# Kernel optimization log

Hardware: AMD Instinct MI355X
Metric: run time of the kernel (lower is better)

Reference implementation:

```python
import jax, jax.numpy as jnp
import numpy as np

B, S, D = 1, 1024, 512
HEADS, HID = 8, 64
DH = D // HEADS          # 64
CD = D * DH              # 32768 channels in diagonal block
DT = 0.1


def causal_fft_conv(u, k):
    # u: (..., C, S), k: (C, S) -> causal convolution along last axis
    s = u.shape[-1]
    n = 2 * s
    Uf = jnp.fft.rfft(u, n=n, axis=-1)
    Kf = jnp.fft.rfft(k, n=n, axis=-1)
    return jnp.fft.irfft(Uf * Kf, n=n, axis=-1)[..., :s]


def setup_inputs() -> dict:
    key = jax.random.key(0)
    ks = jax.random.split(key, 10)
    x = jax.random.normal(ks[0], (B, S, D), dtype=jnp.float32)
    sc = 1.0 / np.sqrt(D)
    WQ = jax.random.normal(ks[1], (D, D), dtype=jnp.float32) * sc
    WK = jax.random.normal(ks[2], (D, D), dtype=jnp.float32) * sc
    WV = jax.random.normal(ks[3], (D, D), dtype=jnp.float32) * sc
    WO = jax.random.normal(ks[4], (D, D), dtype=jnp.float32) * sc
    # shift SSM: taps C (A = shift matrix, B = e1) + skip D
    C_shift = jax.random.normal(ks[5], (D, HID), dtype=jnp.float32) / np.sqrt(HID)
    D_shift = jax.random.normal(ks[6], (D,), dtype=jnp.float32)
    # S4D-Inv initialization (deterministic: real_random=imag_random=False)
    n = np.arange(HID, dtype=np.float32)
    A_re = jnp.full((HID,), -0.5, dtype=jnp.float32)
    A_im = jnp.asarray((HID / np.pi) * (HID / (2.0 * n + 1.0) - 1.0), dtype=jnp.float32)
    C_re = jax.random.normal(ks[7], (CD, HID), dtype=jnp.float32) / np.sqrt(HID)
    C_im = jax.random.normal(ks[8], (CD, HID), dtype=jnp.float32) / np.sqrt(HID)
    D_diag = jax.random.normal(ks[9], (CD,), dtype=jnp.float32)
    return {"x": x, "WQ": WQ, "WK": WK, "WV": WV, "WO": WO,
            "C_shift": C_shift, "D_shift": D_shift,
            "A_re": A_re, "A_im": A_im, "C_re": C_re, "C_im": C_im,
            "D_diag": D_diag}


def reference(x, WQ, WK, WV, WO, C_shift, D_shift, A_re, A_im, C_re, C_im, D_diag):
    b, s, d = x.shape
    Q = x @ WQ.T
    K = x @ WK.T
    V = x @ WV.T

    # ---- S4 shift block on K: FIR conv with taps C_shift + skip ----
    k_shift = jnp.pad(C_shift, ((0, 0), (0, s - HID)))  # (D, S)
    Kc = jnp.swapaxes(K, 1, 2)                          # (B, D, S)
    Kc = causal_fft_conv(Kc, k_shift) + D_shift[:, None] * Kc
    K = jnp.swapaxes(Kc, 1, 2)

    # ---- heads ----
    Qh = jnp.swapaxes(Q.reshape(b, s, HEADS, DH), 1, 2)  # (B,H,S,dh)
    Kh = jnp.swapaxes(K.reshape(b, s, HEADS, DH), 1, 2)
    Vh = jnp.swapaxes(V.reshape(b, s, HEADS, DH), 1, 2)

    # KV outer product: (B,H,S,dh,dh)
    KV = Kh[..., :, None] * Vh[..., None, :]
    KVf = jnp.transpose(KV, (0, 2, 1, 3, 4)).reshape(b, s, CD)

    # ---- S4D diagonal block (bilinear disc., convolutional form) ----
    A = A_re + 1j * A_im                                # (N,) complex
    dA = (1.0 + DT * A / 2.0) / (1.0 - DT * A / 2.0)
    dB = DT / (1.0 - DT * A / 2.0)
    logdA = jnp.log(dA)                                 # (N,)
    vand = jnp.exp(jnp.arange(s)[None, :] * logdA[:, None])  # (N, S)
    CB = (C_re + 1j * C_im) * dB[None, :]               # (CD, N)
    Kd = 2.0 * jnp.real(CB @ vand)                      # (CD, S) SSM kernel

    KVc = jnp.swapaxes(KVf, 1, 2)                       # (B, CD, S)
    KVc = causal_fft_conv(KVc, Kd) + D_diag[:, None] * KVc
    KVd = jnp.swapaxes(KVc, 1, 2).reshape(b, s, HEADS, DH, DH)
    KVd = jnp.transpose(KVd, (0, 2, 1, 3, 4))           # (B,H,S,dh,dh)

    # ---- combine with Q and output projection ----
    O = jnp.einsum('bhnc,bhncd->bhnd', Qh, KVd)         # (B,H,S,dh)
    O = jnp.swapaxes(O, 1, 2).reshape(b, s, d)
    return O @ WO.T
```

## Files before the change

### kernel.cpp

```cpp
#include <hip/hip_runtime.h>

#define S 1024
#define D 512
#define HID 64
#define CD 32768
#define DT 0.1f

typedef __attribute__((ext_vector_type(4))) float floatx4;
typedef __attribute__((ext_vector_type(8))) short shortx8;
typedef short shortx8_a __attribute__((ext_vector_type(8), may_alias));
typedef short shortx4_a __attribute__((ext_vector_type(4), may_alias));
typedef unsigned int uint_a __attribute__((may_alias));
typedef unsigned int uint2_a __attribute__((ext_vector_type(2), may_alias));
typedef float float4_a __attribute__((ext_vector_type(4), may_alias));
typedef float float_a __attribute__((may_alias));

__device__ __forceinline__ unsigned short f2bf(float f) {
  union { float f; unsigned int u; } v;
  v.f = f;
  unsigned int r = v.u + 0x7FFFu + ((v.u >> 16) & 1u);
  return (unsigned short)(r >> 16);
}
__device__ __forceinline__ float bf2f(unsigned short h) {
  union { unsigned int u; float f; } v;
  v.u = ((unsigned int)h) << 16;
  return v.f;
}
__device__ __forceinline__ void cvt_hilo(float v, unsigned short& h, unsigned short& lo) {
  h = f2bf(v);
  lo = f2bf(v - bf2f(h));
}

__global__ __launch_bounds__(256) void fused_qkv_cbkd(
    const float* __restrict__ x, const float* __restrict__ WQ,
    const float* __restrict__ WK, const float* __restrict__ WV,
    const float* __restrict__ Are, const float* __restrict__ Aim,
    const float* __restrict__ Cre, const float* __restrict__ Cim,
    float* __restrict__ QT, float* __restrict__ KrawT, float* __restrict__ VT,
    unsigned short* __restrict__ cb2pack, unsigned short* __restrict__ kdpack) {
  __shared__ __align__(16) char LB[21760];
  const int tid = threadIdx.x;
  const int bid = blockIdx.x;
  const int l = tid & 63, w = tid >> 6;
  const int l15 = l & 15, q = l >> 4;

  if (bid < 384) {
    unsigned short* Wh = (unsigned short*)LB;
    unsigned short* Wl = Wh + 2560;
    unsigned short* Xh = Wl + 2560;
    unsigned short* Xl = Xh + 2560;
    float_a* Ct = (float_a*)LB;
    const int mat = bid >> 7;
    const int rem = bid & 127;
    const int n0 = (rem & 7) * 64, m0 = (rem >> 3) * 64;
    const float* Wsel = (mat == 0) ? WQ : (mat == 1) ? WK : WV;
    float* CT = (mat == 0) ? QT : (mat == 1) ? KrawT : VT;

    floatx4 acc[4];
#pragma unroll
    for (int nt = 0; nt < 4; ++nt) acc[nt] = (floatx4){0.f, 0.f, 0.f, 0.f};

    for (int k0 = 0; k0 < D; k0 += 32) {
      if (k0) __syncthreads();
#pragma unroll
      for (int p = 0; p < 2; ++p) {
        const int idx = tid + 256 * p;
        const int row = idx >> 3, c4 = (idx & 7) * 4;
        const float4 wv = *(const float4*)&Wsel[(n0 + row) * D + k0 + c4];
        const float4 xv = *(const float4*)&x[(m0 + row) * D + k0 + c4];
        unsigned short h0, h1, h2, h3, g0, g1, g2, g3;
        cvt_hilo(wv.x, h0, g0); cvt_hilo(wv.y, h1, g1);
        cvt_hilo(wv.z, h2, g2); cvt_hilo(wv.w, h3, g3);
        uint2_a hv = {(unsigned int)h0 | ((unsigned int)h1 << 16),
                      (unsigned int)h2 | ((unsigned int)h3 << 16)};
        uint2_a lv = {(unsigned int)g0 | ((unsigned int)g1 << 16),
                      (unsigned int)g2 | ((unsigned int)g3 << 16)};
        *(uint2_a*)&Wh[row * 40 + c4] = hv;
        *(uint2_a*)&Wl[row * 40 + c4] = lv;
        cvt_hilo(xv.x, h0, g0); cvt_hilo(xv.y, h1, g1);
        cvt_hilo(xv.z, h2, g2); cvt_hilo(xv.w, h3, g3);
        uint2_a hv2 = {(unsigned int)h0 | ((unsigned int)h1 << 16),
                       (unsigned int)h2 | ((unsigned int)h3 << 16)};
        uint2_a lv2 = {(unsigned int)g0 | ((unsigned int)g1 << 16),
                       (unsigned int)g2 | ((unsigned int)g3 << 16)};
        *(uint2_a*)&Xh[row * 40 + c4] = hv2;
        *(uint2_a*)&Xl[row * 40 + c4] = lv2;
      }
      __syncthreads();
      const shortx8 xh = *(const shortx8_a*)&Xh[(16 * w + l15) * 40 + 8 * q];
      const shortx8 xl = *(const shortx8_a*)&Xl[(16 * w + l15) * 40 + 8 * q];
#pragma unroll
      for (int nt = 0; nt < 4; ++nt) {
        const shortx8 wh = *(const shortx8_a*)&Wh[(16 * nt + l15) * 40 + 8 * q];
        const shortx8 wl = *(const shortx8_a*)&Wl[(16 * nt + l15) * 40 + 8 * q];
        acc[nt] = __builtin_amdgcn_mfma_f32_16x16x32_bf16(wh, xh, acc[nt], 0, 0, 0);
        acc[nt] = __builtin_amdgcn_mfma_f32_16x16x32_bf16(wh, xl, acc[nt], 0, 0, 0);
        acc[nt] = __builtin_amdgcn_mfma_f32_16x16x32_bf16(wl, xh, acc[nt], 0, 0, 0);
      }
    }
    __syncthreads();
#pragma unroll
    for (int nt = 0; nt < 4; ++nt)
#pragma unroll
      for (int v = 0; v < 4; ++v)
        Ct[(16 * nt + 4 * q + v) * 68 + 16 * w + l15] = acc[nt][v];
    __syncthreads();
#pragma unroll
    for (int p = 0; p < 4; ++p) {
      const int row = (tid >> 4) + 16 * p;
      const int col4 = (tid & 15) * 4;
      *(float4_a*)&CT[(n0 + row) * S + m0 + col4] = *(const float4_a*)&Ct[row * 68 + col4];
    }
  } else {
    unsigned short* cbs = (unsigned short*)LB;
    unsigned short* PCc2s = (unsigned short*)(LB + 4352);
    const int c0 = (bid - 384) << 4;
    {
      const int n = l, seg = w;
      const float ar = Are[n], ai = Aim[n];
      const float den_re = 1.0f - 0.05f * ar;
      const float den_im = -0.05f * ai;
      const float num_re = 1.0f + 0.05f * ar;
      const float num_im = 0.05f * ai;
      const float inv_d2 = 1.0f / (den_re * den_re + den_im * den_im);
      const float dAr = (num_re * den_re + num_im * den_im) * inv_d2;
      const float dAi = (num_im * den_re - num_re * den_im) * inv_d2;
      float e2r = dAr * dAr - dAi * dAi, e2i = 2.0f * dAr * dAi;
      float e4r = e2r * e2r - e2i * e2i, e4i = 2.0f * e2r * e2i;
      float e8r = e4r * e4r - e4i * e4i, e8i = 2.0f * e4r * e4i;
      float e16r = e8r * e8r - e8i * e8i, e16i = 2.0f * e8r * e8i;
      float br = 1.0f, bi = 0.0f;
      for (int sgo = 0; sgo < seg; ++sgo) {
        const float nr = br * e16r - bi * e16i;
        bi = br * e16i + bi * e16r;
        br = nr;
      }
      float pr = br, pi = bi;
      for (int k = 16 * seg + 1; k <= 16 * seg + 16; ++k) {
        const float nr = pr * dAr - pi * dAi;
        pi = pr * dAi + pi * dAr;
        pr = nr;
        if (k <= 63) {
          PCc2s[k * 136 + n] = f2bf(pr);
          PCc2s[k * 136 + 64 + n] = f2bf(-pi);
        }
      }
      if (seg == 0) {
        PCc2s[n] = f2bf(1.0f);
        PCc2s[64 + n] = 0;
      }
    }
#pragma unroll
    for (int ii = 0; ii < 4; ++ii) {
      const int idx = tid + 256 * ii;
      const int ci = idx >> 6, n = idx & 63;
      const int c = c0 + ci;
      const float ar = Are[n], ai = Aim[n];
      const float den_re = 1.0f - 0.05f * ar;
      const float den_im = -0.05f * ai;
      const float inv_d2 = 1.0f / (den_re * den_re + den_im * den_im);
      const float dBr = DT * den_re * inv_d2;
      const float dBi = -DT * den_im * inv_d2;
      const float cr = Cre[c * HID + n], cim = Cim[c * HID + n];
      const unsigned short re = f2bf(2.0f * (cr * dBr - cim * dBi));
      const unsigned short im = f2bf(2.0f * (cr * dBi + cim * dBr));
      cbs[ci * 136 + n] = re;
      cbs[ci * 136 + 64 + n] = im;
      cb2pack[c * 128 + n] = re;
      cb2pack[c * 128 + 64 + n] = im;
    }
    __syncthreads();
    floatx4 acc = {0.f, 0.f, 0.f, 0.f};
#pragma unroll
    for (int k = 0; k < 4; ++k) {
      const shortx8 a = *(const shortx8_a*)&cbs[l15 * 136 + 8 * q + 32 * k];
      const shortx8 b = *(const shortx8_a*)&PCc2s[(16 * w + l15) * 136 + 8 * q + 32 * k];
      acc = __builtin_amdgcn_mfma_f32_16x16x32_bf16(a, b, acc, 0, 0, 0);
    }
    const int dlt = 16 * w + l15;
#pragma unroll
    for (int v = 0; v < 4; ++v)
      kdpack[(c0 + 4 * q + v) * 128 + 64 - dlt] = f2bf(acc[v]);
    const int row = tid >> 4, p = tid & 15;
#pragma unroll
    for (int k2 = 0; k2 < 4; ++k2) {
      const int idx = p + 16 * k2;
      const int m = (idx == 0) ? 0 : 64 + idx;
      kdpack[(c0 + row) * 128 + m] = 0;
    }
  }
}

__global__ __launch_bounds__(256) void shift_ssmT(const float* __restrict__ KrawT,
                                                  const float* __restrict__ Cs,
                                                  const float* __restrict__ Ds,
                                                  float* __restrict__ KnT) {
  __shared__ float kpad[64 + S];
  const int d = blockIdx.x, tid = threadIdx.x;
  if (tid < 64) kpad[tid] = 0.0f;
  *(float4_a*)&kpad[64 + 4 * tid] = *(const float4_a*)&KrawT[d * S + 4 * tid];
  const float dskip = Ds[d];
  const float* taps = Cs + d * HID;
  __syncthreads();
  float acc[4];
#pragma unroll
  for (int s = 0; s < 4; ++s) acc[s] = dskip * kpad[64 + tid + 256 * s];
  for (int j = 0; j < 64; ++j) {
    const float tj = taps[j];
#pragma unroll
    for (int s = 0; s < 4; ++s) acc[s] += tj * kpad[64 + tid + 256 * s - j];
  }
#pragma unroll
  for (int s = 0; s < 4; ++s) KnT[d * S + tid + 256 * s] = acc[s];
}

__global__ __launch_bounds__(256) void s4d_fused(
    const float* __restrict__ KnT, const float* __restrict__ VT,
    const float* __restrict__ QT,
    const float* __restrict__ Are, const float* __restrict__ Aim,
    const unsigned short* __restrict__ cb2pack,
    const unsigned short* __restrict__ kdpack,
    const float* __restrict__ Dd, float* __restrict__ OT) {
  __shared__ __align__(16) unsigned short SHu[34368];
  const int tid = threadIdx.x;
  const int l = tid & 63, w = tid >> 6;
  const int l15 = l & 15, q = l >> 4;
  const int h = blockIdx.x >> 6, j = blockIdx.x & 63;
  const int dv = (h << 6) + j;

  {
    const int n = l, seg = w;
    unsigned short* PAreW = SHu;
    unsigned short* PAimW = SHu + 4608;
    unsigned short* PCcW = SHu + 9216;
    float_a* dA64W = (float_a*)(SHu + 17920);
    const float ar = Are[n], ai = Aim[n];
    const float den_re = 1.0f - 0.05f * ar;
    const float den_im = -0.05f * ai;
    const float num_re = 1.0f + 0.05f * ar;
    const float num_im = 0.05f * ai;
    const float inv_d2 = 1.0f / (den_re * den_re + den_im * den_im);
    const float dAr = (num_re * den_re + num_im * den_im) * inv_d2;
    const float dAi = (num_im * den_re - num_re * den_im) * inv_d2;
    float e2r = dAr * dAr - dAi * dAi, e2i = 2.0f * dAr * dAi;
    float e4r = e2r * e2r - e2i * e2i, e4i = 2.0f * e2r * e2i;
    float e8r = e4r * e4r - e4i * e4i, e8i = 2.0f * e4r * e4i;
    float e16r = e8r * e8r - e8i * e8i, e16i = 2.0f * e8r * e8i;
    float br = 1.0f, bi = 0.0f;
    for (int sgo = 0; sgo < seg; ++sgo) {
      const float nr = br * e16r - bi * e16i;
      bi = br * e16i + bi * e16r;
      br = nr;
    }
    float pr = br, pi = bi;
    for (int k = 16 * seg + 1; k <= 16 * seg + 16; ++k) {
      const float nr = pr * dAr - pi * dAi;
      pi = pr * dAi + pi * dAr;
      pr = nr;
      if (k <= 63) {
        PAreW[n * 72 + 63 - k] = f2bf(pr);
        PAimW[n * 72 + 63 - k] = f2bf(pi);
      }
      PCcW[(k - 1) * 136 + n] = f2bf(pr);
      PCcW[(k - 1) * 136 + 64 + n] = f2bf(-pi);
      if (k == 64) {
        dA64W[2 * n] = pr;
        dA64W[2 * n + 1] = pi;
      }
    }
    if (seg == 0) {
      PAreW[n * 72 + 63] = f2bf(1.0f);
      PAimW[n * 72 + 63] = 0;
    }
  }
  float4 vvr[4];
#pragma unroll
  for (int s = 0; s < 4; ++s)
    vvr[s] = *(const float4*)&VT[dv * S + 4 * l + 256 * s];

  float4 kx[4], qtv[4];
  float c2r, c2i, dd;
  unsigned int kdv;
  {
    const int i = w;
    const int dk = (h << 6) + i;
    const int c = (h << 12) + (i << 6) + j;
    const int kb = dk * S + 4 * l;
#pragma unroll
    for (int s = 0; s < 4; ++s) {
      kx[s] = *(const float4*)&KnT[kb + 256 * s];
      qtv[s] = *(const float4*)&QT[kb + 256 * s];
    }
    c2r = bf2f(cb2pack[c * 128 + l]);
    c2i = bf2f(cb2pack[c * 128 + 64 + l]);
    kdv = *(const uint_a*)&kdpack[c * 128 + 2 * l];
    dd = Dd[c];
  }
  __syncthreads();

  const unsigned short* PAre = SHu;
  const unsigned short* PAim = SHu + 4608;
  const unsigned short* PCc = SHu + 9216;
  const float_a* dA64v = (const float_a*)(SHu + 17920);
  unsigned short* WB = SHu + 18176 + w * 4048;
  unsigned short* Ub = WB;
  unsigned short* SXY = WB + 1152;
  uint_a* kdR32 = (uint_a*)(WB + 3328);
  unsigned short* kdSH = WB + 3472;
  float_a* yf = (float_a*)SXY;

  const float er = dA64v[2 * l], ei = dA64v[2 * l + 1];
  float4 Oa[4];
#pragma unroll
  for (int s = 0; s < 4; ++s) Oa[s] = make_float4(0.f, 0.f, 0.f, 0.f);

#pragma unroll 1
  for (int it = 0; it < 16; ++it) {
    float4 nkx[4], nqt[4];
    float nc2r = 0.f, nc2i = 0.f, ndd = 0.f;
    unsigned int nkdv = 0;
    if (it < 15) {
      const int i = (it + 1) * 4 + w;
      const int dk = (h << 6) + i;
      const int c = (h << 12) + (i << 6) + j;
      const int kb = dk * S + 4 * l;
#pragma unroll
      for (int s = 0; s < 4; ++s) {
        nkx[s] = *(const float4*)&KnT[kb + 256 * s];
        nqt[s] = *(const float4*)&QT[kb + 256 * s];
      }
      nc2r = bf2f(cb2pack[c * 128 + l]);
      nc2i = bf2f(cb2pack[c * 128 + 64 + l]);
      nkdv = *(const uint_a*)&kdpack[c * 128 + 2 * l];
      ndd = Dd[c];
    }

#pragma unroll
    for (int s = 0; s < 4; ++s) {
      const int t = 4 * l + 256 * s;
      const int g = t >> 6, r = t & 63;
      uint2_a pp;
      pp.x = (unsigned int)f2bf(kx[s].x * vvr[s].x) | ((unsigned int)f2bf(kx[s].y * vvr[s].y) << 16);
      pp.y = (unsigned int)f2bf(kx[s].z * vvr[s].z) | ((unsigned int)f2bf(kx[s].w * vvr[s].w) << 16);
      *(uint2_a*)&Ub[g * 72 + r] = pp;
    }
    kdR32[l] = kdv;
    if (l < 4) kdR32[64 + l] = 0;
    asm volatile("" ::: "memory");
#pragma unroll
    for (int s2 = 0; s2 < 4; ++s2) {
      unsigned int v;
      if (s2 == 0) {
        v = kdR32[l];
      } else if (s2 == 1) {
        v = (kdR32[l] >> 16) | (kdR32[l + 1] << 16);
      } else if (s2 == 2) {
        v = kdR32[l + 1];
      } else {
        v = (kdR32[l + 1] >> 16) | (kdR32[l + 2] << 16);
      }
      *(uint_a*)&kdSH[s2 * 136 + 2 * l] = v;
    }
    asm volatile("" ::: "memory");
    const shortx8 b0 = *(const shortx8_a*)&Ub[l15 * 72 + 8 * q];
    const shortx8 b1 = *(const shortx8_a*)&Ub[l15 * 72 + 8 * q + 32];
#pragma unroll
    for (int tt = 0; tt < 4; ++tt) {
      const int rowb = (tt * 16 + l15) * 72 + 8 * q;
      const shortx8 ar0 = *(const shortx8_a*)&PAre[rowb];
      const shortx8 ar1 = *(const shortx8_a*)&PAre[rowb + 32];
      const shortx8 ai0 = *(const shortx8_a*)&PAim[rowb];
      const shortx8 ai1 = *(const shortx8_a*)&PAim[rowb + 32];
      floatx4 z = {0.f, 0.f, 0.f, 0.f};
      floatx4 sre = __builtin_amdgcn_mfma_f32_16x16x32_bf16(ar0, b0, z, 0, 0, 0);
      sre = __builtin_amdgcn_mfma_f32_16x16x32_bf16(ar1, b1, sre, 0, 0, 0);
      floatx4 sim = __builtin_amdgcn_mfma_f32_16x16x32_bf16(ai0, b0, z, 0, 0, 0);
      sim = __builtin_amdgcn_mfma_f32_16x16x32_bf16(ai1, b1, sim, 0, 0, 0);
      const int sb = l15 * 136 + tt * 16 + 4 * q;
      *(uint_a*)&SXY[sb] = (unsigned int)f2bf(sre[0]) | ((unsigned int)f2bf(sre[1]) << 16);
      *(uint_a*)&SXY[sb + 2] = (unsigned int)f2bf(sre[2]) | ((unsigned int)f2bf(sre[3]) << 16);
      *(uint_a*)&SXY[sb + 64] = (unsigned int)f2bf(sim[0]) | ((unsigned int)f2bf(sim[1]) << 16);
      *(uint_a*)&SXY[sb + 66] = (unsigned int)f2bf(sim[2]) | ((unsigned int)f2bf(sim[3]) << 16);
    }
    asm volatile("" ::: "memory");
    {
      float srr[16], sii[16];
#pragma unroll
      for (int g = 0; g < 16; ++g) {
        srr[g] = bf2f(SXY[g * 136 + l]);
        sii[g] = bf2f(SXY[g * 136 + 64 + l]);
      }
      float xr = 0.f, xi = 0.f;
#pragma unroll
      for (int g = 0; g < 16; ++g) {
        SXY[g * 136 + l] = f2bf(c2r * xr - c2i * xi);
        SXY[g * 136 + 64 + l] = f2bf(c2r * xi + c2i * xr);
        const float nr = er * xr - ei * xi + srr[g];
        xi = er * xi + ei * xr + sii[g];
        xr = nr;
      }
    }
    asm volatile("" ::: "memory");
    floatx4 acc[4];
#pragma unroll
    for (int tt = 0; tt < 4; ++tt) acc[tt] = (floatx4){0.f, 0.f, 0.f, 0.f};
#pragma unroll
    for (int k = 0; k < 4; ++k) {
      const shortx8 xa = *(const shortx8_a*)&SXY[l15 * 136 + 8 * q + 32 * k];
#pragma unroll
      for (int tt = 0; tt < 4; ++tt) {
        const shortx8 pb = *(const shortx8_a*)&PCc[(tt * 16 + l15) * 136 + 8 * q + 32 * k];
        acc[tt] = __builtin_amdgcn_mfma_f32_16x16x32_bf16(xa, pb, acc[tt], 0, 0, 0);
      }
    }
#pragma unroll
    for (int k = 0; k < 2; ++k) {
      const shortx8 ua = (k == 0) ? b0 : b1;
#pragma unroll
      for (int tt = 0; tt < 4; ++tt) {
        const int r = tt * 16 + l15;
        const int sSh = (4 - (r & 3)) & 3;
        const int addr = sSh * 136 + (64 - r - sSh) + 8 * q + 32 * k;
        const shortx4_a lo = *(const shortx4_a*)&kdSH[addr];
        const shortx4_a hi = *(const shortx4_a*)&kdSH[addr + 4];
        const shortx8 kb8 = __builtin_shufflevector(lo, hi, 0, 1, 2, 3, 4, 5, 6, 7);
        acc[tt] = __builtin_amdgcn_mfma_f32_16x16x32_bf16(ua, kb8, acc[tt], 0, 0, 0);
      }
    }
#pragma unroll
    for (int tt = 0; tt < 4; ++tt) {
      const int r = tt * 16 + l15;
#pragma unroll
      for (int v = 0; v < 4; ++v) {
        const int g = 4 * q + v;
        yf[g * 68 + r] = acc[tt][v] + dd * bf2f(Ub[g * 72 + r]);
      }
    }
    asm volatile("" ::: "memory");
#pragma unroll
    for (int s = 0; s < 4; ++s) {
      const int t = 4 * l + 256 * s;
      const float4_a y4 = *(const float4_a*)&yf[(t >> 6) * 68 + (t & 63)];
      Oa[s].x += qtv[s].x * y4.x;
      Oa[s].y += qtv[s].y * y4.y;
      Oa[s].z += qtv[s].z * y4.z;
      Oa[s].w += qtv[s].w * y4.w;
    }
    asm volatile("" ::: "memory");
#pragma unroll
    for (int s = 0; s < 4; ++s) { kx[s] = nkx[s]; qtv[s] = nqt[s]; }
    c2r = nc2r; c2i = nc2i; kdv = nkdv; dd = ndd;
  }

  {
    float_a* Ow = (float_a*)WB;
#pragma unroll
    for (int s = 0; s < 4; ++s) {
      float4_a vv = {Oa[s].x, Oa[s].y, Oa[s].z, Oa[s].w};
      *(float4_a*)&Ow[4 * l + 256 * s] = vv;
    }
  }
  __syncthreads();
  {
    const int tq = 256 * w + 4 * l;
    float4_a acc = {0.f, 0.f, 0.f, 0.f};
#pragma unroll
    for (int w2 = 0; w2 < 4; ++w2) {
      const float_a* Ow2 = (const float_a*)(SHu + 18176 + w2 * 4048);
      acc += *(const float4_a*)&Ow2[tq];
    }
    *(float4_a*)&OT[dv * S + tq] = acc;
  }
}

__global__ __launch_bounds__(256) void gemm_outT(const float* __restrict__ OT,
                                                 const float* __restrict__ WO,
                                                 float* __restrict__ out) {
  __shared__ __align__(16) char LB[20480];
  unsigned short* Wh = (unsigned short*)LB;
  unsigned short* Wl = Wh + 2560;
  unsigned short* Xh = Wl + 2560;
  unsigned short* Xl = Xh + 2560;
  float_a* Ct = (float_a*)LB;
  const int tid = threadIdx.x;
  const int l = tid & 63, w = tid >> 6;
  const int l15 = l & 15, q = l >> 4;
  const int n0 = (blockIdx.x & 7) * 64, m0 = (blockIdx.x >> 3) * 64;

  floatx4 acc[4];
#pragma unroll
  for (int nt = 0; nt < 4; ++nt) acc[nt] = (floatx4){0.f, 0.f, 0.f, 0.f};

  for (int k0 = 0; k0 < D; k0 += 32) {
    if (k0) __syncthreads();
#pragma unroll
    for (int p = 0; p < 2; ++p) {
      const int idx = tid + 256 * p;
      {
        const int row = idx >> 3, c4 = (idx & 7) * 4;
        const float4 wv = *(const float4*)&WO[(n0 + row) * D + k0 + c4];
        unsigned short h0, h1, h2, h3, g0, g1, g2, g3;
        cvt_hilo(wv.x, h0, g0); cvt_hilo(wv.y, h1, g1);
        cvt_hilo(wv.z, h2, g2); cvt_hilo(wv.w, h3, g3);
        uint2_a hv = {(unsigned int)h0 | ((unsigned int)h1 << 16),
                      (unsigned int)h2 | ((unsigned int)h3 << 16)};
        uint2_a lv = {(unsigned int)g0 | ((unsigned int)g1 << 16),
                      (unsigned int)g2 | ((unsigned int)g3 << 16)};
        *(uint2_a*)&Wh[row * 40 + c4] = hv;
        *(uint2_a*)&Wl[row * 40 + c4] = lv;
      }
      {
        const int kk = idx >> 4, m4 = (idx & 15) * 4;
        const float4 ov = *(const float4*)&OT[(k0 + kk) * S + m0 + m4];
        unsigned short h, g;
        cvt_hilo(ov.x, h, g); Xh[(m4 + 0) * 40 + kk] = h; Xl[(m4 + 0) * 40 + kk] = g;
        cvt_hilo(ov.y, h, g); Xh[(m4 + 1) * 40 + kk] = h; Xl[(m4 + 1) * 40 + kk] = g;
        cvt_hilo(ov.z, h, g); Xh[(m4 + 2) * 40 + kk] = h; Xl[(m4 + 2) * 40 + kk] = g;
        cvt_hilo(ov.w, h, g); Xh[(m4 + 3) * 40 + kk] = h; Xl[(m4 + 3) * 40 + kk] = g;
      }
    }
    __syncthreads();
    const shortx8 xh = *(const shortx8_a*)&Xh[(16 * w + l15) * 40 + 8 * q];
    const shortx8 xl = *(const shortx8_a*)&Xl[(16 * w + l15) * 40 + 8 * q];
#pragma unroll
    for (int nt = 0; nt < 4; ++nt) {
      const shortx8 wh = *(const shortx8_a*)&Wh[(16 * nt + l15) * 40 + 8 * q];
      const shortx8 wl = *(const shortx8_a*)&Wl[(16 * nt + l15) * 40 + 8 * q];
      acc[nt] = __builtin_amdgcn_mfma_f32_16x16x32_bf16(wh, xh, acc[nt], 0, 0, 0);
      acc[nt] = __builtin_amdgcn_mfma_f32_16x16x32_bf16(wh, xl, acc[nt], 0, 0, 0);
      acc[nt] = __builtin_amdgcn_mfma_f32_16x16x32_bf16(wl, xh, acc[nt], 0, 0, 0);
    }
  }
  __syncthreads();
#pragma unroll
  for (int nt = 0; nt < 4; ++nt)
#pragma unroll
    for (int v = 0; v < 4; ++v)
      Ct[(16 * w + l15) * 68 + 16 * nt + 4 * q + v] = acc[nt][v];
  __syncthreads();
#pragma unroll
  for (int p = 0; p < 4; ++p) {
    const int row = (tid >> 4) + 16 * p;
    const int col4 = (tid & 15) * 4;
    *(float4_a*)&out[(m0 + row) * D + n0 + col4] = *(const float4_a*)&Ct[row * 68 + col4];
  }
}

extern "C" void kernel_launch(void* const* d_in, const int* in_sizes, int n_in,
                              void* d_out, int out_size, void* d_ws, size_t ws_size,
                              hipStream_t stream) {
  const float* x   = (const float*)d_in[0];
  const float* WQ  = (const float*)d_in[1];
  const float* WK  = (const float*)d_in[2];
  const float* WV  = (const float*)d_in[3];
  const float* WO  = (const float*)d_in[4];
  const float* Cs  = (const float*)d_in[5];
  const float* Ds  = (const float*)d_in[6];
  const float* Are = (const float*)d_in[7];
  const float* Aim = (const float*)d_in[8];
  const float* Cre = (const float*)d_in[9];
  const float* Cim = (const float*)d_in[10];
  const float* Dd  = (const float*)d_in[11];
  float* out = (float*)d_out;

  char* ws = (char*)d_ws;
  const size_t SD = (size_t)S * D * 4;
  float* QT    = (float*)(ws + 0 * SD);
  float* KrawT = (float*)(ws + 1 * SD);
  float* VT    = (float*)(ws + 2 * SD);
  float* KnT   = (float*)(ws + 3 * SD);
  float* OT    = (float*)(ws + 4 * SD);
  unsigned short* cb2pack = (unsigned short*)(ws + 5 * SD);
  unsigned short* kdpack  = (unsigned short*)(ws + 5 * SD + 8388608);

  fused_qkv_cbkd<<<384 + CD / 16, 256, 0, stream>>>(
      x, WQ, WK, WV, Are, Aim, Cre, Cim, QT, KrawT, VT, cb2pack, kdpack);
  shift_ssmT<<<512, 256, 0, stream>>>(KrawT, Cs, Ds, KnT);
  s4d_fused<<<512, 256, 0, stream>>>(KnT, VT, QT, Are, Aim, cb2pack, kdpack, Dd, OT);
  gemm_outT<<<128, 256, 0, stream>>>(OT, WO, out);
}
```

Measured before the change: 204.9 us.

## Interleave complex LDS layout and accumulate Q product in MFMA registers

```diff
diff --git a/kernel.cpp b/kernel.cpp
--- a/kernel.cpp
+++ b/kernel.cpp
@@ -12,6 +12,7 @@
 typedef short shortx4_a __attribute__((ext_vector_type(4), may_alias));
 typedef unsigned int uint_a __attribute__((may_alias));
 typedef unsigned int uint2_a __attribute__((ext_vector_type(2), may_alias));
+typedef unsigned int uint4_a __attribute__((ext_vector_type(4), may_alias));
 typedef float float4_a __attribute__((ext_vector_type(4), may_alias));
 typedef float float_a __attribute__((may_alias));
 
@@ -214,7 +215,7 @@
   for (int s = 0; s < 4; ++s) KnT[d * S + tid + 256 * s] = acc[s];
 }
 
-__global__ __launch_bounds__(256) void s4d_fused(
+__global__ __launch_bounds__(256, 2) void s4d_fused(
     const float* __restrict__ KnT, const float* __restrict__ VT,
     const float* __restrict__ QT,
     const float* __restrict__ Are, const float* __restrict__ Aim,
@@ -261,8 +262,8 @@
         PAreW[n * 72 + 63 - k] = f2bf(pr);
         PAimW[n * 72 + 63 - k] = f2bf(pi);
       }
-      PCcW[(k - 1) * 136 + n] = f2bf(pr);
-      PCcW[(k - 1) * 136 + 64 + n] = f2bf(-pi);
+      PCcW[(k - 1) * 136 + 2 * n] = f2bf(pr);
+      PCcW[(k - 1) * 136 + 2 * n + 1] = f2bf(-pi);
       if (k == 64) {
         dA64W[2 * n] = pr;
         dA64W[2 * n + 1] = pi;
@@ -278,7 +279,7 @@
   for (int s = 0; s < 4; ++s)
     vvr[s] = *(const float4*)&VT[dv * S + 4 * l + 256 * s];
 
-  float4 kx[4], qtv[4];
+  float4 kx[4];
   float c2r, c2i, dd;
   unsigned int kdv;
   {
@@ -287,10 +288,7 @@
     const int c = (h << 12) + (i << 6) + j;
     const int kb = dk * S + 4 * l;
 #pragma unroll
-    for (int s = 0; s < 4; ++s) {
-      kx[s] = *(const float4*)&KnT[kb + 256 * s];
-      qtv[s] = *(const float4*)&QT[kb + 256 * s];
-    }
+    for (int s = 0; s < 4; ++s) kx[s] = *(const float4*)&KnT[kb + 256 * s];
     c2r = bf2f(cb2pack[c * 128 + l]);
     c2i = bf2f(cb2pack[c * 128 + 64 + l]);
     kdv = *(const uint_a*)&kdpack[c * 128 + 2 * l];
@@ -307,16 +305,32 @@
   unsigned short* SXY = WB + 1152;
   uint_a* kdR32 = (uint_a*)(WB + 3328);
   unsigned short* kdSH = WB + 3472;
-  float_a* yf = (float_a*)SXY;
 
   const float er = dA64v[2 * l], ei = dA64v[2 * l + 1];
-  float4 Oa[4];
-#pragma unroll
-  for (int s = 0; s < 4; ++s) Oa[s] = make_float4(0.f, 0.f, 0.f, 0.f);
+  floatx4 OaccD[4];
+  float4 Odd[4];
+#pragma unroll
+  for (int tt = 0; tt < 4; ++tt) OaccD[tt] = (floatx4){0.f, 0.f, 0.f, 0.f};
+#pragma unroll
+  for (int s = 0; s < 4; ++s) Odd[s] = make_float4(0.f, 0.f, 0.f, 0.f);
 
 #pragma unroll 1
   for (int it = 0; it < 16; ++it) {
-    float4 nkx[4], nqt[4];
+    const int dk_cur = (h << 6) + it * 4 + w;
+    float4 qtv[4];
+    float qD[16];
+    {
+      const int kb = dk_cur * S + 4 * l;
+#pragma unroll
+      for (int s = 0; s < 4; ++s) qtv[s] = *(const float4*)&QT[kb + 256 * s];
+      const int qb = dk_cur * S + 256 * q + l15;
+#pragma unroll
+      for (int tt = 0; tt < 4; ++tt)
+#pragma unroll
+        for (int v = 0; v < 4; ++v)
+          qD[4 * tt + v] = QT[qb + 64 * v + 16 * tt];
+    }
+    float4 nkx[4];
     float nc2r = 0.f, nc2i = 0.f, ndd = 0.f;
     unsigned int nkdv = 0;
     if (it < 15) {
@@ -325,10 +339,7 @@
       const int c = (h << 12) + (i << 6) + j;
       const int kb = dk * S + 4 * l;
 #pragma unroll
-      for (int s = 0; s < 4; ++s) {
-        nkx[s] = *(const float4*)&KnT[kb + 256 * s];
-        nqt[s] = *(const float4*)&QT[kb + 256 * s];
-      }
+      for (int s = 0; s < 4; ++s) nkx[s] = *(const float4*)&KnT[kb + 256 * s];
       nc2r = bf2f(cb2pack[c * 128 + l]);
       nc2i = bf2f(cb2pack[c * 128 + 64 + l]);
       nkdv = *(const uint_a*)&kdpack[c * 128 + 2 * l];
@@ -376,27 +387,29 @@
       sre = __builtin_amdgcn_mfma_f32_16x16x32_bf16(ar1, b1, sre, 0, 0, 0);
       floatx4 sim = __builtin_amdgcn_mfma_f32_16x16x32_bf16(ai0, b0, z, 0, 0, 0);
       sim = __builtin_amdgcn_mfma_f32_16x16x32_bf16(ai1, b1, sim, 0, 0, 0);
-      const int sb = l15 * 136 + tt * 16 + 4 * q;
-      *(uint_a*)&SXY[sb] = (unsigned int)f2bf(sre[0]) | ((unsigned int)f2bf(sre[1]) << 16);
-      *(uint_a*)&SXY[sb + 2] = (unsigned int)f2bf(sre[2]) | ((unsigned int)f2bf(sre[3]) << 16);
-      *(uint_a*)&SXY[sb + 64] = (unsigned int)f2bf(sim[0]) | ((unsigned int)f2bf(sim[1]) << 16);
-      *(uint_a*)&SXY[sb + 66] = (unsigned int)f2bf(sim[2]) | ((unsigned int)f2bf(sim[3]) << 16);
+      uint4_a wv;
+      wv[0] = (unsigned int)f2bf(sre[0]) | ((unsigned int)f2bf(sim[0]) << 16);
+      wv[1] = (unsigned int)f2bf(sre[1]) | ((unsigned int)f2bf(sim[1]) << 16);
+      wv[2] = (unsigned int)f2bf(sre[2]) | ((unsigned int)f2bf(sim[2]) << 16);
+      wv[3] = (unsigned int)f2bf(sre[3]) | ((unsigned int)f2bf(sim[3]) << 16);
+      *(uint4_a*)&SXY[l15 * 136 + 32 * tt + 8 * q] = wv;
     }
     asm volatile("" ::: "memory");
     {
-      float srr[16], sii[16];
+      unsigned int rdv[16];
+#pragma unroll
+      for (int g = 0; g < 16; ++g) rdv[g] = *(const uint_a*)&SXY[g * 136 + 2 * l];
+      float xr = 0.f, xi = 0.f;
 #pragma unroll
       for (int g = 0; g < 16; ++g) {
-        srr[g] = bf2f(SXY[g * 136 + l]);
-        sii[g] = bf2f(SXY[g * 136 + 64 + l]);
-      }
-      float xr = 0.f, xi = 0.f;
-#pragma unroll
-      for (int g = 0; g < 16; ++g) {
-        SXY[g * 136 + l] = f2bf(c2r * xr - c2i * xi);
-        SXY[g * 136 + 64 + l] = f2bf(c2r * xi + c2i * xr);
-        const float nr = er * xr - ei * xi + srr[g];
-        xi = er * xi + ei * xr + sii[g];
+        *(uint_a*)&SXY[g * 136 + 2 * l] =
+            (unsigned int)f2bf(c2r * xr - c2i * xi) |
+            ((unsigned int)f2bf(c2r * xi + c2i * xr) << 16);
+        union { unsigned int u; float f; } lo, hi;
+        lo.u = rdv[g] << 16;
+        hi.u = rdv[g] & 0xffff0000u;
+        const float nr = er * xr - ei * xi + lo.f;
+        xi = er * xi + ei * xr + hi.f;
         xr = nr;
       }
     }
@@ -428,36 +441,45 @@
       }
     }
 #pragma unroll
-    for (int tt = 0; tt < 4; ++tt) {
-      const int r = tt * 16 + l15;
-#pragma unroll
-      for (int v = 0; v < 4; ++v) {
-        const int g = 4 * q + v;
-        yf[g * 68 + r] = acc[tt][v] + dd * bf2f(Ub[g * 72 + r]);
-      }
-    }
+    for (int tt = 0; tt < 4; ++tt)
+#pragma unroll
+      for (int v = 0; v < 4; ++v)
+        OaccD[tt][v] += qD[4 * tt + v] * acc[tt][v];
+#pragma unroll
+    for (int s = 0; s < 4; ++s) {
+      Odd[s].x += dd * qtv[s].x * (kx[s].x * vvr[s].x);
+      Odd[s].y += dd * qtv[s].y * (kx[s].y * vvr[s].y);
+      Odd[s].z += dd * qtv[s].z * (kx[s].z * vvr[s].z);
+      Odd[s].w += dd * qtv[s].w * (kx[s].w * vvr[s].w);
+    }
+#pragma unroll
+    for (int s = 0; s < 4; ++s) kx[s] = nkx[s];
+    c2r = nc2r; c2i = nc2i; kdv = nkdv; dd = ndd;
+  }
+
+  asm volatile("" ::: "memory");
+  {
+    float_a* Ored = (float_a*)WB;
+#pragma unroll
+    for (int tt = 0; tt < 4; ++tt)
+#pragma unroll
+      for (int v = 0; v < 4; ++v)
+        Ored[256 * q + 64 * v + 16 * tt + l15 + q] = OaccD[tt][v];
     asm volatile("" ::: "memory");
+    float4 Oa[4];
 #pragma unroll
     for (int s = 0; s < 4; ++s) {
-      const int t = 4 * l + 256 * s;
-      const float4_a y4 = *(const float4_a*)&yf[(t >> 6) * 68 + (t & 63)];
-      Oa[s].x += qtv[s].x * y4.x;
-      Oa[s].y += qtv[s].y * y4.y;
-      Oa[s].z += qtv[s].z * y4.z;
-      Oa[s].w += qtv[s].w * y4.w;
+      const float4_a y4 = *(const float4_a*)&Ored[4 * l + 257 * s];
+      Oa[s].x = y4.x + Odd[s].x;
+      Oa[s].y = y4.y + Odd[s].y;
+      Oa[s].z = y4.z + Odd[s].z;
+      Oa[s].w = y4.w + Odd[s].w;
     }
     asm volatile("" ::: "memory");
-#pragma unroll
-    for (int s = 0; s < 4; ++s) { kx[s] = nkx[s]; qtv[s] = nqt[s]; }
-    c2r = nc2r; c2i = nc2i; kdv = nkdv; dd = ndd;
-  }
-
-  {
-    float_a* Ow = (float_a*)WB;
 #pragma unroll
     for (int s = 0; s < 4; ++s) {
       float4_a vv = {Oa[s].x, Oa[s].y, Oa[s].z, Oa[s].w};
-      *(float4_a*)&Ow[4 * l + 256 * s] = vv;
+      *(float4_a*)&Ored[4 * l + 256 * s] = vv;
     }
   }
   __syncthreads();
```

Measured after the change: 189.5 us. -7.5%, faster.
